# Kernel tuning notes

Hardware: AMD Instinct MI355X
Metric: run time of the kernel (lower is better)

The kernel has to match this reference:

```python
import jax, jax.numpy as jnp
import numpy as np

# Quantization constants from the original module
X_SCALE, X_ZP = 0.0215, -25
Y_SCALE, Y_ZP = 0.0176, 18


def setup_inputs() -> dict:
    key = jax.random.key(0)
    kx, ky = jax.random.split(key)
    K, N = 8192, 16384
    # int8 stand-ins (enum lacks int8); values fit int8 range
    x = jax.random.randint(kx, (K,), 0, 127, dtype=jnp.int32)
    y = jax.random.randint(ky, (K, N), 0, 127, dtype=jnp.int32)
    return {"x": x, "y": y}


def reference(x, y):
    # dequantize_per_tensor: (q - zero_point) * scale, in fp32
    xf = (x.astype(jnp.float32) - X_ZP) * X_SCALE   # [K]
    yf = (y.astype(jnp.float32) - Y_ZP) * Y_SCALE   # [K, N]
    # vector-matrix matmul -> [N]
    return xf @ yf
```

## Files before the change

### kernel.cpp

```cpp
#include <hip/hip_runtime.h>


constexpr int K = 8192;
constexpr int N = 16384;
constexpr float X_SCALE = 0.0215f;
constexpr int   X_ZP    = -25;
constexpr float Y_SCALE = 0.0176f;
constexpr int   Y_ZP    = 18;

constexpr int BLOCK = 256;
constexpr int VEC   = 4;
constexpr int COLS_PER_BLOCK = BLOCK * VEC;
constexpr int NBLK_N = N / COLS_PER_BLOCK;
constexpr int SPLIT_K = 128;
constexpr int KCHUNK = K / SPLIT_K;
constexpr int N4 = N / 4;

typedef int ivec4 __attribute__((ext_vector_type(4)));

__global__ __launch_bounds__(BLOCK, 8) void qgemv_partial(const int* __restrict__ x,
                                                          const ivec4* __restrict__ y,
                                                          ivec4* __restrict__ ws) {
    __shared__ int xs[KCHUNK];

    const int nb = blockIdx.x % NBLK_N;
    const int kc = blockIdx.x / NBLK_N;
    const int k0 = kc * KCHUNK;

    if (threadIdx.x < KCHUNK)
        xs[threadIdx.x] = x[k0 + threadIdx.x] - X_ZP;
    __syncthreads();

    const int col4 = nb * (COLS_PER_BLOCK / 4) + threadIdx.x;
    const ivec4* yv = y + (size_t)k0 * N4 + col4;

    const int r0 = (13 * kc + 7 * nb) & (KCHUNK - 1);

    int acc0 = 0, acc1 = 0, acc2 = 0, acc3 = 0;
    int sx = 0;

#pragma unroll 8
    for (int i = 0; i < KCHUNK; ++i) {
        int k = r0 + i;
        if (k >= KCHUNK) k -= KCHUNK;
        ivec4 v = __builtin_nontemporal_load(&yv[(size_t)k * N4]);
        int a = xs[k];
        sx   += a;
        acc0 += a * v.x;
        acc1 += a * v.y;
        acc2 += a * v.z;
        acc3 += a * v.w;
    }

    const int corr = Y_ZP * sx;
    ivec4 p;
    p.x = acc0 - corr;
    p.y = acc1 - corr;
    p.z = acc2 - corr;
    p.w = acc3 - corr;
    ws[(size_t)kc * N4 + col4] = p;
}

__global__ __launch_bounds__(BLOCK) void qgemv_reduce(const ivec4* __restrict__ ws,
                                                      float* __restrict__ out) {
    const int t = blockIdx.x * BLOCK + threadIdx.x;
    int sx = 0, sy = 0, sz = 0, sw = 0;
#pragma unroll 8
    for (int kc = 0; kc < SPLIT_K; ++kc) {
        ivec4 v = ws[(size_t)kc * N4 + t];
        sx += v.x; sy += v.y; sz += v.z; sw += v.w;
    }
    const float s = X_SCALE * Y_SCALE;
    float4 o;
    o.x = s * (float)sx;
    o.y = s * (float)sy;
    o.z = s * (float)sz;
    o.w = s * (float)sw;
    ((float4*)out)[t] = o;
}

extern "C" void kernel_launch(void* const* d_in, const int* in_sizes, int n_in,
                              void* d_out, int out_size, void* d_ws, size_t ws_size,
                              hipStream_t stream) {
    const int* x = (const int*)d_in[0];
    const ivec4* y = (const ivec4*)d_in[1];
    float* out = (float*)d_out;
    ivec4* ws = (ivec4*)d_ws;

    qgemv_partial<<<NBLK_N * SPLIT_K, BLOCK, 0, stream>>>(x, y, ws);
    qgemv_reduce<<<N4 / BLOCK, BLOCK, 0, stream>>>(ws, out);
}
```

Baseline: 656.3 us.

## Restructure GEMV so each block covers full row span with 16 K rows

The partial kernel now launches one block per K-chunk of 16 rows. Each thread loads 16 strided ivec4 columns per row and keeps 16 vector accumulators in registers, instead of one block per 1024-column tile over 64 rows. This gives more independent loads in flight per thread and reads whole contiguous rows of y. The partial-sum workspace grows to 512 slices, so the reduction is split into two stages. The risks are high register pressure, only 512 blocks for the GPU, and more workspace traffic.

```diff
diff --git a/kernel.cpp b/kernel.cpp
--- a/kernel.cpp
+++ b/kernel.cpp
@@ -8,66 +8,89 @@
 constexpr float Y_SCALE = 0.0176f;
 constexpr int   Y_ZP    = 18;
 
-constexpr int BLOCK = 256;
-constexpr int VEC   = 4;
-constexpr int COLS_PER_BLOCK = BLOCK * VEC;
-constexpr int NBLK_N = N / COLS_PER_BLOCK;
-constexpr int SPLIT_K = 128;
-constexpr int KCHUNK = K / SPLIT_K;
-constexpr int N4 = N / 4;
+constexpr int BLOCK   = 256;
+constexpr int N4      = N / 4;
+constexpr int SPLIT_K = 512;
+constexpr int KCHUNK  = K / SPLIT_K;
+constexpr int JVEC    = N4 / BLOCK;
+constexpr int RED1      = 16;
+constexpr int RED1_SPAN = SPLIT_K / RED1;
 
 typedef int ivec4 __attribute__((ext_vector_type(4)));
 
-__global__ __launch_bounds__(BLOCK, 8) void qgemv_partial(const int* __restrict__ x,
+__global__ __launch_bounds__(BLOCK, 2) void qgemv_partial(const int* __restrict__ x,
                                                           const ivec4* __restrict__ y,
                                                           ivec4* __restrict__ ws) {
     __shared__ int xs[KCHUNK];
-
-    const int nb = blockIdx.x % NBLK_N;
-    const int kc = blockIdx.x / NBLK_N;
+    const int kc = blockIdx.x;
     const int k0 = kc * KCHUNK;
 
     if (threadIdx.x < KCHUNK)
         xs[threadIdx.x] = x[k0 + threadIdx.x] - X_ZP;
     __syncthreads();
 
-    const int col4 = nb * (COLS_PER_BLOCK / 4) + threadIdx.x;
-    const ivec4* yv = y + (size_t)k0 * N4 + col4;
+    const int r0 = (kc * 7) & (KCHUNK - 1);
+    const int j0 = (kc * 5) & (JVEC - 1);
 
-    const int r0 = (13 * kc + 7 * nb) & (KCHUNK - 1);
-
-    int acc0 = 0, acc1 = 0, acc2 = 0, acc3 = 0;
+    ivec4 acc[JVEC];
+#pragma unroll
+    for (int j = 0; j < JVEC; ++j) {
+        acc[j].x = 0; acc[j].y = 0; acc[j].z = 0; acc[j].w = 0;
+    }
     int sx = 0;
 
-#pragma unroll 8
-    for (int i = 0; i < KCHUNK; ++i) {
-        int k = r0 + i;
-        if (k >= KCHUNK) k -= KCHUNK;
-        ivec4 v = __builtin_nontemporal_load(&yv[(size_t)k * N4]);
-        int a = xs[k];
-        sx   += a;
-        acc0 += a * v.x;
-        acc1 += a * v.y;
-        acc2 += a * v.z;
-        acc3 += a * v.w;
+#pragma unroll 1
+    for (int rr = 0; rr < KCHUNK; ++rr) {
+        const int r = (r0 + rr) & (KCHUNK - 1);
+        const int a = xs[r];
+        sx += a;
+        const ivec4* __restrict__ yp = y + (size_t)(k0 + r) * N4 + threadIdx.x;
+#pragma unroll
+        for (int jj = 0; jj < JVEC; ++jj) {
+            const int j = (j0 + jj) & (JVEC - 1);
+            const ivec4 v = __builtin_nontemporal_load(&yp[j * BLOCK]);
+            acc[jj].x += a * v.x;
+            acc[jj].y += a * v.y;
+            acc[jj].z += a * v.z;
+            acc[jj].w += a * v.w;
+        }
     }
 
     const int corr = Y_ZP * sx;
-    ivec4 p;
-    p.x = acc0 - corr;
-    p.y = acc1 - corr;
-    p.z = acc2 - corr;
-    p.w = acc3 - corr;
-    ws[(size_t)kc * N4 + col4] = p;
+    ivec4* __restrict__ wp = ws + (size_t)kc * N4 + threadIdx.x;
+#pragma unroll
+    for (int jj = 0; jj < JVEC; ++jj) {
+        const int j = (j0 + jj) & (JVEC - 1);
+        ivec4 p = acc[jj];
+        p.x -= corr; p.y -= corr; p.z -= corr; p.w -= corr;
+        wp[j * BLOCK] = p;
+    }
 }
 
-__global__ __launch_bounds__(BLOCK) void qgemv_reduce(const ivec4* __restrict__ ws,
-                                                      float* __restrict__ out) {
-    const int t = blockIdx.x * BLOCK + threadIdx.x;
+__global__ __launch_bounds__(BLOCK) void qgemv_reduce1(const ivec4* __restrict__ ws,
+                                                       ivec4* __restrict__ ws2) {
+    const int cb = blockIdx.x & (N4 / BLOCK - 1);
+    const int kb = blockIdx.x / (N4 / BLOCK);
+    const int col4 = cb * BLOCK + threadIdx.x;
+    const int kc0 = kb * RED1_SPAN;
     int sx = 0, sy = 0, sz = 0, sw = 0;
 #pragma unroll 8
-    for (int kc = 0; kc < SPLIT_K; ++kc) {
-        ivec4 v = ws[(size_t)kc * N4 + t];
+    for (int i = 0; i < RED1_SPAN; ++i) {
+        ivec4 v = ws[(size_t)(kc0 + i) * N4 + col4];
+        sx += v.x; sy += v.y; sz += v.z; sw += v.w;
+    }
+    ivec4 p;
+    p.x = sx; p.y = sy; p.z = sz; p.w = sw;
+    ws2[(size_t)kb * N4 + col4] = p;
+}
+
+__global__ __launch_bounds__(BLOCK) void qgemv_reduce2(const ivec4* __restrict__ ws2,
+                                                       float* __restrict__ out) {
+    const int col4 = blockIdx.x * BLOCK + threadIdx.x;
+    int sx = 0, sy = 0, sz = 0, sw = 0;
+#pragma unroll
+    for (int kb = 0; kb < RED1; ++kb) {
+        ivec4 v = ws2[(size_t)kb * N4 + col4];
         sx += v.x; sy += v.y; sz += v.z; sw += v.w;
     }
     const float s = X_SCALE * Y_SCALE;
@@ -76,7 +99,7 @@
     o.y = s * (float)sy;
     o.z = s * (float)sz;
     o.w = s * (float)sw;
-    ((float4*)out)[t] = o;
+    ((float4*)out)[col4] = o;
 }
 
 extern "C" void kernel_launch(void* const* d_in, const int* in_sizes, int n_in,
@@ -86,7 +109,9 @@
     const ivec4* y = (const ivec4*)d_in[1];
     float* out = (float*)d_out;
     ivec4* ws = (ivec4*)d_ws;
+    ivec4* ws2 = ws + (size_t)SPLIT_K * N4;
 
-    qgemv_partial<<<NBLK_N * SPLIT_K, BLOCK, 0, stream>>>(x, y, ws);
-    qgemv_reduce<<<N4 / BLOCK, BLOCK, 0, stream>>>(ws, out);
+    qgemv_partial<<<SPLIT_K, BLOCK, 0, stream>>>(x, y, ws);
+    qgemv_reduce1<<<(N4 / BLOCK) * RED1, BLOCK, 0, stream>>>(ws, ws2);
+    qgemv_reduce2<<<N4 / BLOCK, BLOCK, 0, stream>>>(ws2, out);
 }
```

After: 714.3 us. 8.8% more time.

## Interleave split-K rows across blocks and parallelize reduction over K groups

Applied to the files above, without the earlier changes.

The partial kernel now gives each block a strided set of K rows (kb, kb+128, ...) in place of a contiguous chunk with a rotated start offset. Consecutive blocks therefore read adjacent rows at the same time, which should change DRAM page and channel locality. The reduce kernel splits the 128 partial rows across thread groups within a block and combines them through shared memory, giving more memory parallelism than one thread serially summing 128 rows. The cost is an extra sync and a shared-memory combine step in the reduce kernel.

```diff
diff --git a/kernel.cpp b/kernel.cpp
--- a/kernel.cpp
+++ b/kernel.cpp
@@ -8,43 +8,36 @@
 constexpr float Y_SCALE = 0.0176f;
 constexpr int   Y_ZP    = 18;
 
-constexpr int BLOCK = 256;
-constexpr int VEC   = 4;
-constexpr int COLS_PER_BLOCK = BLOCK * VEC;
-constexpr int NBLK_N = N / COLS_PER_BLOCK;
+constexpr int BLOCK  = 256;
+constexpr int N4     = N / 4;
+constexpr int NBLK_N = 16;
 constexpr int SPLIT_K = 128;
-constexpr int KCHUNK = K / SPLIT_K;
-constexpr int N4 = N / 4;
+constexpr int KITER  = K / SPLIT_K;
 
 typedef int ivec4 __attribute__((ext_vector_type(4)));
 
 __global__ __launch_bounds__(BLOCK, 8) void qgemv_partial(const int* __restrict__ x,
                                                           const ivec4* __restrict__ y,
                                                           ivec4* __restrict__ ws) {
-    __shared__ int xs[KCHUNK];
+    __shared__ int xs[KITER];
 
     const int nb = blockIdx.x % NBLK_N;
-    const int kc = blockIdx.x / NBLK_N;
-    const int k0 = kc * KCHUNK;
+    const int kb = blockIdx.x / NBLK_N;
 
-    if (threadIdx.x < KCHUNK)
-        xs[threadIdx.x] = x[k0 + threadIdx.x] - X_ZP;
+    if (threadIdx.x < KITER)
+        xs[threadIdx.x] = x[kb + SPLIT_K * threadIdx.x] - X_ZP;
     __syncthreads();
 
-    const int col4 = nb * (COLS_PER_BLOCK / 4) + threadIdx.x;
-    const ivec4* yv = y + (size_t)k0 * N4 + col4;
-
-    const int r0 = (13 * kc + 7 * nb) & (KCHUNK - 1);
+    const int col4 = nb * (BLOCK) + threadIdx.x;
+    const ivec4* __restrict__ yv = y + (size_t)kb * N4 + col4;
 
     int acc0 = 0, acc1 = 0, acc2 = 0, acc3 = 0;
     int sx = 0;
 
 #pragma unroll 8
-    for (int i = 0; i < KCHUNK; ++i) {
-        int k = r0 + i;
-        if (k >= KCHUNK) k -= KCHUNK;
-        ivec4 v = __builtin_nontemporal_load(&yv[(size_t)k * N4]);
-        int a = xs[k];
+    for (int i = 0; i < KITER; ++i) {
+        ivec4 v = __builtin_nontemporal_load(&yv[(size_t)i * (SPLIT_K * N4)]);
+        int a = xs[i];
         sx   += a;
         acc0 += a * v.x;
         acc1 += a * v.y;
@@ -58,25 +51,46 @@
     p.y = acc1 - corr;
     p.z = acc2 - corr;
     p.w = acc3 - corr;
-    ws[(size_t)kc * N4 + col4] = p;
+    ws[(size_t)kb * N4 + col4] = p;
 }
+
+constexpr int RBLK = 128;
+constexpr int CPB  = N4 / RBLK;
+constexpr int GRP  = BLOCK / CPB;
+constexpr int PER  = SPLIT_K / GRP;
 
 __global__ __launch_bounds__(BLOCK) void qgemv_reduce(const ivec4* __restrict__ ws,
                                                       float* __restrict__ out) {
-    const int t = blockIdx.x * BLOCK + threadIdx.x;
+    __shared__ ivec4 red[GRP][CPB];
+    const int c = threadIdx.x % CPB;
+    const int g = threadIdx.x / CPB;
+    const int col4 = blockIdx.x * CPB + c;
+
     int sx = 0, sy = 0, sz = 0, sw = 0;
-#pragma unroll 8
-    for (int kc = 0; kc < SPLIT_K; ++kc) {
-        ivec4 v = ws[(size_t)kc * N4 + t];
+#pragma unroll
+    for (int i = 0; i < PER; ++i) {
+        ivec4 v = ws[(size_t)(g * PER + i) * N4 + col4];
         sx += v.x; sy += v.y; sz += v.z; sw += v.w;
     }
-    const float s = X_SCALE * Y_SCALE;
-    float4 o;
-    o.x = s * (float)sx;
-    o.y = s * (float)sy;
-    o.z = s * (float)sz;
-    o.w = s * (float)sw;
-    ((float4*)out)[t] = o;
+    ivec4 p; p.x = sx; p.y = sy; p.z = sz; p.w = sw;
+    red[g][c] = p;
+    __syncthreads();
+
+    if (g == 0) {
+        ivec4 t = red[0][c];
+#pragma unroll
+        for (int gg = 1; gg < GRP; ++gg) {
+            ivec4 v = red[gg][c];
+            t.x += v.x; t.y += v.y; t.z += v.z; t.w += v.w;
+        }
+        const float s = X_SCALE * Y_SCALE;
+        float4 o;
+        o.x = s * (float)t.x;
+        o.y = s * (float)t.y;
+        o.z = s * (float)t.z;
+        o.w = s * (float)t.w;
+        ((float4*)out)[col4] = o;
+    }
 }
 
 extern "C" void kernel_launch(void* const* d_in, const int* in_sizes, int n_in,
@@ -87,6 +101,6 @@
     float* out = (float*)d_out;
     ivec4* ws = (ivec4*)d_ws;
 
-    qgemv_partial<<<NBLK_N * SPLIT_K, BLOCK, 0, stream>>>(x, y, ws);
-    qgemv_reduce<<<N4 / BLOCK, BLOCK, 0, stream>>>(ws, out);
+    qgemv_partial<<<SPLIT_K * NBLK_N, BLOCK, 0, stream>>>(x, y, ws);
+    qgemv_reduce<<<RBLK, BLOCK, 0, stream>>>(ws, out);
 }
```

New measurement: 677.2 us. 3.2% more time.
